# Kernel optimization log

Measured on AMD Instinct MI355X. Metric: run time of the kernel, lower is better.

The kernel has to match this reference:

```python
import jax, jax.numpy as jnp
import numpy as np
import math

N = 100000       # nodes
E = 640000       # edges
VOCAB = 8192
EMB = 96         # node_embedding_dim
SEL = 32         # node_selector_dim
H = EMB + SEL    # hidden_dim = 128
T = 3            # num_edge_types
P = 64           # positional_embedding_dim
MAXPOS = 512     # max_edge_position
ITERS = 6        # ggnn_iterations


def _sinusoidal(max_pos, dim):
    pos = np.arange(max_pos)[:, None].astype(np.float32)
    div = np.exp(np.arange(0, dim, 2).astype(np.float32) * (-math.log(10000.0) / dim))
    pe = np.zeros((max_pos, dim), np.float32)
    pe[:, 0::2] = np.sin(pos * div)
    pe[:, 1::2] = np.cos(pos * div)
    return jnp.asarray(pe)


def setup_inputs() -> dict:
    key = jax.random.key(0)
    ks = jax.random.split(key, 20)
    s = 1.0 / np.sqrt(H).astype(np.float32)
    inp = {
        "x_text_indices": jax.random.randint(ks[0], (N,), 0, VOCAB, dtype=jnp.int32),
        "node_selectors": jax.random.normal(ks[1], (N, SEL), jnp.float32),
        "edge_index": jax.random.randint(ks[2], (2, E), 0, N, dtype=jnp.int32),
        "edge_type": jax.random.randint(ks[3], (E,), 0, T, dtype=jnp.int32),
        "edge_positions": jax.random.randint(ks[4], (E,), 0, MAXPOS + 1, dtype=jnp.int32),
        "emb": (jax.random.normal(ks[5], (VOCAB, EMB), jnp.float32) * 0.02).at[0].set(0.0),  # padding_idx=0
        "pos_enc": _sinusoidal(MAXPOS + 1, P),
        "Wg": jax.random.normal(ks[6], (P, H), jnp.float32) * (1.0 / np.sqrt(P)),
        "bg": jnp.zeros((H,), jnp.float32),
        "Wt": jax.random.normal(ks[7], (T, H, H), jnp.float32) * s,
        "bt": jnp.zeros((T, H), jnp.float32),
        "W_ih": jax.random.normal(ks[8], (3 * H, H), jnp.float32) * s,
        "W_hh": jax.random.normal(ks[9], (3 * H, H), jnp.float32) * s,
        "b_ih": jnp.zeros((3 * H,), jnp.float32),
        "b_hh": jnp.zeros((3 * H,), jnp.float32),
        "W1": jax.random.normal(ks[10], (2 * H, H), jnp.float32) * (1.0 / np.sqrt(2 * H)),
        "b1": jnp.zeros((H,), jnp.float32),
        "W2": jax.random.normal(ks[11], (H, 1), jnp.float32) * s,
        "b2": jnp.zeros((1,), jnp.float32),
    }
    return inp


def _gru_cell(x, h, W_ih, W_hh, b_ih, b_hh):
    # torch.nn.GRUCell math
    gi = x @ W_ih.T + b_ih          # [N, 3H]
    gh = h @ W_hh.T + b_hh          # [N, 3H]
    i_r, i_z, i_n = jnp.split(gi, 3, axis=-1)
    h_r, h_z, h_n = jnp.split(gh, 3, axis=-1)
    r = jax.nn.sigmoid(i_r + h_r)
    z = jax.nn.sigmoid(i_z + h_z)
    n = jnp.tanh(i_n + r * h_n)
    return (1.0 - z) * n + z * h


def reference(x_text_indices, node_selectors, edge_index, edge_type, edge_positions,
              emb, pos_enc, Wg, bg, Wt, bt, W_ih, W_hh, b_ih, b_hh, W1, b1, W2, b2):
    src, dst = edge_index[0], edge_index[1]
    h0 = jnp.concatenate([emb[x_text_indices], node_selectors], axis=-1)  # [N, H]
    pe_e = pos_enc[edge_positions]                                        # [E, P]
    gate = 2.0 * jax.nn.sigmoid(pe_e @ Wg + bg)                           # [E, H]
    cnt = jax.ops.segment_sum(jnp.ones((E,), h0.dtype), dst, num_segments=N)
    denom = jnp.maximum(cnt, 1.0)[:, None]                                # mean-scatter, 0 if no in-edges

    h = h0
    for _ in range(ITERS):
        gx = h[src] * gate                                                # gather + gate [E, H]
        # edge-type routed linear: sum over the one active type per edge
        msg = jnp.zeros_like(gx)
        for t in range(T):
            mask = (edge_type == t)[:, None].astype(gx.dtype)
            msg = msg + mask * (gx @ Wt[t] + bt[t])
        agg = jax.ops.segment_sum(msg, dst, num_segments=N) / denom       # mean aggregation [N, H]
        h = _gru_cell(agg, h, W_ih, W_hh, b_ih, b_hh)

    feats = jnp.concatenate([h, h0], axis=-1)                             # [N, 2H]
    logits = jax.nn.relu(feats @ W1 + b1) @ W2 + b2                       # [N, 1]
    return logits
```

## Files before the change

### kernel.cpp

```cpp
#include <hip/hip_runtime.h>
#include <cstdint>
#include <cstddef>

#define HD 128
#define EMBD 96
#define SELD 32
#define PD 64
#define NPOS 513
#define GITERS 6

typedef _Float16 f16;
typedef __attribute__((ext_vector_type(8))) _Float16 f16x8;
typedef __attribute__((ext_vector_type(4))) _Float16 f16x4;
typedef __attribute__((ext_vector_type(2))) _Float16 f16x2;
typedef __attribute__((ext_vector_type(4))) float f32x4;

__device__ __forceinline__ float sigm(float x) {
    return __builtin_amdgcn_rcpf(1.0f + __expf(-x));
}
__device__ __forceinline__ float tanh_f(float x) {
    return 2.0f * __builtin_amdgcn_rcpf(1.0f + __expf(-2.0f * x)) - 1.0f;
}


__global__ void k_deg(const int* __restrict__ ei, const int* __restrict__ et,
                      int* __restrict__ cnt_t, int E, int N) {
    int e = blockIdx.x * 256 + threadIdx.x;
    if (e < E) {
        int d = ei[E + e];
        atomicAdd(&cnt_t[(size_t)et[e] * N + d], 1);
    }
}

__launch_bounds__(1024)
__global__ void k_scan1(const int* __restrict__ cnt_t, int* __restrict__ rp,
                        int* __restrict__ bsum, int N) {
    __shared__ int sc[1024];
    int t = threadIdx.x;
    int i = blockIdx.x * 1024 + t;
    int v = 0;
    if (i < N)
        v = cnt_t[i] + cnt_t[(size_t)N + i] + cnt_t[2 * (size_t)N + i];
    sc[t] = v;
    __syncthreads();
    for (int off = 1; off < 1024; off <<= 1) {
        int u = (t >= off) ? sc[t - off] : 0;
        __syncthreads();
        sc[t] += u;
        __syncthreads();
    }
    if (i < N) rp[i] = sc[t] - v;
    if (t == 1023) bsum[blockIdx.x] = sc[t];
}

__launch_bounds__(1024)
__global__ void k_scan2(int* __restrict__ bsum, int nb) {
    __shared__ int sc[1024];
    int t = threadIdx.x;
    int v = (t < nb) ? bsum[t] : 0;
    sc[t] = v;
    __syncthreads();
    for (int off = 1; off < 1024; off <<= 1) {
        int u = (t >= off) ? sc[t - off] : 0;
        __syncthreads();
        sc[t] += u;
        __syncthreads();
    }
    if (t < nb) bsum[t] = sc[t] - v;
}

__global__ void k_scan3(const int* __restrict__ rp, const int* __restrict__ bsum,
                        const int* __restrict__ cnt_t, float4* __restrict__ cntp,
                        int4* __restrict__ rp4, int N) {
    int i = blockIdx.x * 256 + threadIdx.x;
    if (i < N) {
        int start = rp[i] + bsum[i >> 10];
        int c0 = cnt_t[i];
        int c1 = cnt_t[(size_t)N + i];
        int c2 = cnt_t[2 * (size_t)N + i];
        rp4[i] = make_int4(start, start + c0, start + c0 + c1, start + c0 + c1 + c2);
        float4 v;
        v.x = (float)c0; v.y = (float)c1; v.z = (float)c2;
        v.w = 1.0f / fmaxf((float)(c0 + c1 + c2), 1.0f);
        cntp[i] = v;
    }
}

__global__ void k_fill(const int* __restrict__ ei, const int* __restrict__ et,
                       const int* __restrict__ ep, const int4* __restrict__ rp4,
                       int* __restrict__ cur3, int2* __restrict__ e2, int E, int N) {
    int e = blockIdx.x * 256 + threadIdx.x;
    if (e < E) {
        int d = ei[E + e];
        int t = et[e];
        int4 r4 = rp4[d];
        int base = (t == 0) ? r4.x : ((t == 1) ? r4.y : r4.z);
        int pos = atomicAdd(&cur3[(size_t)t * N + d], 1);
        e2[base + pos] = make_int2(ei[e], ep[e]);
    }
}

__global__ void k_gate(const float* __restrict__ pe, const float* __restrict__ Wg,
                       const float* __restrict__ bg, f16* __restrict__ gb) {
    int p = blockIdx.x;
    int j = threadIdx.x;
    float acc = bg[j];
    #pragma unroll 8
    for (int k = 0; k < PD; ++k) acc += pe[p * PD + k] * Wg[k * HD + j];
    gb[p * HD + j] = (f16)(2.0f * sigm(acc));
}

__global__ void k_prep(const float* __restrict__ Wt, const float* __restrict__ W1,
                       f16* __restrict__ WtT, f16* __restrict__ W1T) {
    const int SZ = 3 * HD * HD;
    int id = blockIdx.x * 256 + threadIdx.x;
    if (id < SZ) {
        int t = id / (HD * HD), rem = id % (HD * HD);
        int n = rem / HD, k = rem % HD;
        WtT[id] = (f16)Wt[t * HD * HD + k * HD + n];
    } else if (id < SZ + 2 * HD * HD) {
        int rem = id - SZ;
        int n = rem / (2 * HD), k = rem % (2 * HD);
        W1T[rem] = (f16)W1[k * HD + n];
    }
}

__global__ void k_prepW(const float* __restrict__ Wih, const float* __restrict__ Whh,
                        f16* __restrict__ Wcat) {
    int id = blockIdx.x * 256 + threadIdx.x;
    if (id < 512 * 256) {
        int j = id >> 8, k = id & 255;
        float v;
        if (j < 256)      v = (k < 128) ? Wih[j * 128 + k] : Whh[j * 128 + (k - 128)];
        else if (j < 384) v = (k < 128) ? Wih[j * 128 + k] : 0.0f;
        else              v = (k < 128) ? 0.0f : Whh[(j - 128) * 128 + (k - 128)];
        Wcat[id] = (f16)v;
    }
}

__global__ void k_init(const int* __restrict__ xidx, const float* __restrict__ sel,
                       const float* __restrict__ emb, f16* __restrict__ h, int N) {
    int id = blockIdx.x * 256 + threadIdx.x;
    if (id < N * HD) {
        int n = id >> 7, j = id & 127;
        float v = (j < EMBD) ? emb[(size_t)xidx[n] * EMBD + j]
                             : sel[(size_t)n * SELD + (j - EMBD)];
        h[id] = (f16)v;
    }
}

__launch_bounds__(512, 4)
__global__ void k_agg(const int4* __restrict__ rp4, const int2* __restrict__ e2,
                      const f16* __restrict__ h_in, const f16* __restrict__ gb,
                      const f16* __restrict__ WtT, const float* __restrict__ bt,
                      const float4* __restrict__ cntp, f16* __restrict__ agg, int N) {
    __shared__ f16 S[3 * 16 * 136];
    __shared__ f16 aggL[16 * 136];

    int tid = threadIdx.x;
    int wave = tid >> 6, lane = tid & 63;
    int quad = lane >> 4, m = lane & 15;
    int half = lane >> 5, hl = lane & 31;
    int d0 = blockIdx.x * 16;

    {
        int lrow = wave + half * 8;
        int grow = d0 + lrow;
        bool valid = grow < N;
        int4 r4 = rp4[min(grow, N - 1)];
        int es = r4.x, b1 = r4.y, b2 = r4.z, ee = r4.w;
        if (!valid) ee = es;
        int dg = ee - es;
        int dmax = max(dg, __shfl_xor(dg, 32));
        int nb = (__builtin_amdgcn_readfirstlane(dmax) + 7) >> 3;
        int co = hl * 4;

        const f16x4 zf = {0, 0, 0, 0};
        f16x4 accA = zf, accB = zf, accC = zf;
        for (int b = 0; b < nb; ++b) {
            int e0 = es + b * 8;
            int2 ev[8];
            #pragma unroll
            for (int j = 0; j < 8; ++j) {
                int idx = max(min(e0 + j, ee - 1), 0);
                ev[j] = e2[idx];
            }
            f16x4 hv[8], gv[8];
            #pragma unroll
            for (int j = 0; j < 8; ++j) {
                hv[j] = *(const f16x4*)(h_in + (size_t)ev[j].x * HD + co);
                gv[j] = *(const f16x4*)(gb + (size_t)ev[j].y * HD + co);
            }
            #pragma unroll
            for (int j = 0; j < 8; ++j) {
                int eidx = e0 + j;
                f16x4 g0 = (eidx < ee) ? gv[j] : zf;
                accA += hv[j] * g0;
                f16x4 gB = (eidx >= b1) ? g0 : zf;
                accB += hv[j] * gB;
                f16x4 gC = (eidx >= b2) ? g0 : zf;
                accC += hv[j] * gC;
            }
        }
        f16x4 s0 = accA - accB;
        f16x4 s1 = accB - accC;
        *(f16x4*)(S + (0 * 16 + lrow) * 136 + co) = s0;
        *(f16x4*)(S + (1 * 16 + lrow) * 136 + co) = s1;
        *(f16x4*)(S + (2 * 16 + lrow) * 136 + co) = accC;
    }
    __syncthreads();

    {
        int col = wave * 16 + m;
        f32x4 acc = {0.f, 0.f, 0.f, 0.f};
        #pragma unroll
        for (int t = 0; t < 3; ++t)
            #pragma unroll
            for (int c = 0; c < 4; ++c) {
                f16x8 a = *(const f16x8*)(S + (t * 16 + m) * 136 + c * 32 + quad * 8);
                f16x8 b = *(const f16x8*)(WtT + ((size_t)t * HD + col) * HD + c * 32 + quad * 8);
                acc = __builtin_amdgcn_mfma_f32_16x16x32_f16(a, b, acc, 0, 0, 0);
            }
        float bt0 = bt[col], bt1 = bt[HD + col], bt2 = bt[2 * HD + col];
        #pragma unroll
        for (int r = 0; r < 4; ++r) {
            int lr = quad * 4 + r;
            int dd2 = min(d0 + lr, N - 1);
            float4 cp = cntp[dd2];
            float v = (acc[r] + cp.x * bt0 + cp.y * bt1 + cp.z * bt2) * cp.w;
            aggL[lr * 136 + col] = (f16)v;
        }
    }
    __syncthreads();

    {
        int row = tid >> 5, ch = tid & 31;
        if (d0 + row < N) {
            f16x4 v = *(const f16x4*)(aggL + row * 136 + ch * 4);
            *(f16x4*)(agg + (size_t)(d0 + row) * HD + ch * 4) = v;
        }
    }
}

__launch_bounds__(512, 4)
__global__ void k_gru(const f16* __restrict__ agg, const f16* __restrict__ h_in,
                      const f16* __restrict__ Wcat, const float* __restrict__ bih,
                      const float* __restrict__ bhh, f16* __restrict__ h_out, int N) {
    __shared__ f16 AL[64 * 264];

    int tid = threadIdx.x;
    int wave = tid >> 6, lane = tid & 63;
    int quad = lane >> 4, m = lane & 15;
    int d0 = blockIdx.x * 64;

    {
        int rsub = tid >> 5;
        int ch = tid & 31;
        #pragma unroll
        for (int i = 0; i < 4; ++i) {
            int row = i * 16 + rsub;
            int grow = min(d0 + row, N - 1);
            f16x8 v;
            if (ch < 16) v = *(const f16x8*)(agg + (size_t)grow * HD + ch * 8);
            else         v = *(const f16x8*)(h_in + (size_t)grow * HD + (ch - 16) * 8);
            *(f16x8*)(AL + row * 264 + ch * 8) = v;
        }
    }
    __syncthreads();

    int j = wave * 16 + m;
    f32x4 ar[4], az[4], an[4], ah[4];
    const f32x4 z4 = {0.f, 0.f, 0.f, 0.f};
    #pragma unroll
    for (int tau = 0; tau < 4; ++tau) { ar[tau] = z4; az[tau] = z4; an[tau] = z4; ah[tau] = z4; }

    #pragma unroll
    for (int c = 0; c < 8; ++c) {
        f16x8 br = *(const f16x8*)(Wcat + (size_t)j * 256 + c * 32 + quad * 8);
        f16x8 bz = *(const f16x8*)(Wcat + (size_t)(128 + j) * 256 + c * 32 + quad * 8);
        f16x8 bn = (c < 4)
            ? *(const f16x8*)(Wcat + (size_t)(256 + j) * 256 + c * 32 + quad * 8)
            : *(const f16x8*)(Wcat + (size_t)(384 + j) * 256 + c * 32 + quad * 8);
        #pragma unroll
        for (int tau = 0; tau < 4; ++tau) {
            f16x8 a = *(const f16x8*)(AL + (tau * 16 + m) * 264 + c * 32 + quad * 8);
            ar[tau] = __builtin_amdgcn_mfma_f32_16x16x32_f16(a, br, ar[tau], 0, 0, 0);
            az[tau] = __builtin_amdgcn_mfma_f32_16x16x32_f16(a, bz, az[tau], 0, 0, 0);
            if (c < 4) an[tau] = __builtin_amdgcn_mfma_f32_16x16x32_f16(a, bn, an[tau], 0, 0, 0);
            else       ah[tau] = __builtin_amdgcn_mfma_f32_16x16x32_f16(a, bn, ah[tau], 0, 0, 0);
        }
    }

    float b_r  = bih[j] + bhh[j];
    float b_z  = bih[HD + j] + bhh[HD + j];
    float b_in = bih[2 * HD + j];
    float b_hn = bhh[2 * HD + j];
    float hp[4][4];
    #pragma unroll
    for (int tau = 0; tau < 4; ++tau)
        #pragma unroll
        for (int r = 0; r < 4; ++r) {
            int row = tau * 16 + quad * 4 + r;
            float hval = (float)AL[row * 264 + 128 + j];
            float rr = sigm(ar[tau][r] + b_r);
            float zz = sigm(az[tau][r] + b_z);
            float nn = tanh_f(an[tau][r] + b_in + rr * (ah[tau][r] + b_hn));
            hp[tau][r] = (1.0f - zz) * nn + zz * hval;
        }
    __syncthreads();

    #pragma unroll
    for (int tau = 0; tau < 4; ++tau)
        #pragma unroll
        for (int r = 0; r < 4; ++r)
            AL[(tau * 16 + quad * 4 + r) * 132 + j] = (f16)hp[tau][r];
    __syncthreads();

    {
        int rsub = tid >> 5, ch = tid & 31;
        #pragma unroll
        for (int i = 0; i < 4; ++i) {
            int row = i * 16 + rsub;
            if (d0 + row < N) {
                f16x4 v = *(const f16x4*)(AL + row * 132 + ch * 4);
                *(f16x4*)(h_out + (size_t)(d0 + row) * HD + ch * 4) = v;
            }
        }
    }
}

__launch_bounds__(256)
__global__ void k_final(const f16* __restrict__ h_f, const int* __restrict__ xidx,
                        const float* __restrict__ sel, const float* __restrict__ emb,
                        const f16* __restrict__ W1T, const float* __restrict__ b1,
                        const float* __restrict__ W2, const float* __restrict__ b2,
                        float* __restrict__ out, int N) {
    __shared__ float red[4][16];
    int tid = threadIdx.x;
    int wave = tid >> 6, lane = tid & 63;
    int quad = lane >> 4, m = lane & 15;
    int row0 = blockIdx.x * 16;
    int arow = min(row0 + m, N - 1);
    int xi = xidx[arow];

    f16x8 fa[8];
    #pragma unroll
    for (int c = 0; c < 4; ++c)
        fa[c] = *(const f16x8*)(h_f + (size_t)arow * HD + c * 32 + quad * 8);
    #pragma unroll
    for (int c = 4; c < 7; ++c) {
        const float* ep = emb + (size_t)xi * EMBD + (c - 4) * 32 + quad * 8;
        #pragma unroll
        for (int jj = 0; jj < 8; ++jj) fa[c][jj] = (f16)ep[jj];
    }
    {
        const float* sp = sel + (size_t)arow * SELD + quad * 8;
        #pragma unroll
        for (int jj = 0; jj < 8; ++jj) fa[7][jj] = (f16)sp[jj];
    }

    f32x4 acc[2];
    const f32x4 z4 = {0.f, 0.f, 0.f, 0.f};
    acc[0] = z4; acc[1] = z4;
    #pragma unroll
    for (int s = 0; s < 2; ++s) {
        int c0 = (wave * 2 + s) * 16;
        #pragma unroll
        for (int c = 0; c < 8; ++c) {
            f16x8 b = *(const f16x8*)(W1T + (size_t)(c0 + m) * (2 * HD) + c * 32 + quad * 8);
            acc[s] = __builtin_amdgcn_mfma_f32_16x16x32_f16(fa[c], b, acc[s], 0, 0, 0);
        }
    }

    float psum[4] = {0.f, 0.f, 0.f, 0.f};
    #pragma unroll
    for (int s = 0; s < 2; ++s) {
        int col = (wave * 2 + s) * 16 + m;
        float b1v = b1[col], w2v = W2[col];
        #pragma unroll
        for (int r = 0; r < 4; ++r)
            psum[r] += fmaxf(acc[s][r] + b1v, 0.0f) * w2v;
    }
    #pragma unroll
    for (int off = 1; off < 16; off <<= 1)
        #pragma unroll
        for (int r = 0; r < 4; ++r) psum[r] += __shfl_xor(psum[r], off);

    if (m == 0) {
        #pragma unroll
        for (int r = 0; r < 4; ++r) red[wave][quad * 4 + r] = psum[r];
    }
    __syncthreads();
    if (tid < 16) {
        int row = row0 + tid;
        if (row < N) out[row] = red[0][tid] + red[1][tid] + red[2][tid] + red[3][tid] + b2[0];
    }
}


extern "C" void kernel_launch(void* const* d_in, const int* in_sizes, int n_in,
                              void* d_out, int out_size, void* d_ws, size_t ws_size,
                              hipStream_t stream) {
    const int*   xidx = (const int*)d_in[0];
    const float* sel  = (const float*)d_in[1];
    const int*   ei   = (const int*)d_in[2];
    const int*   et   = (const int*)d_in[3];
    const int*   ep   = (const int*)d_in[4];
    const float* emb  = (const float*)d_in[5];
    const float* pe   = (const float*)d_in[6];
    const float* Wg   = (const float*)d_in[7];
    const float* bg   = (const float*)d_in[8];
    const float* Wt   = (const float*)d_in[9];
    const float* bt   = (const float*)d_in[10];
    const float* Wih  = (const float*)d_in[11];
    const float* Whh  = (const float*)d_in[12];
    const float* bih  = (const float*)d_in[13];
    const float* bhh  = (const float*)d_in[14];
    const float* W1   = (const float*)d_in[15];
    const float* b1   = (const float*)d_in[16];
    const float* W2   = (const float*)d_in[17];
    const float* b2   = (const float*)d_in[18];

    const int N = in_sizes[0];
    const int E = in_sizes[3];
    const size_t NH = (size_t)N * HD;

    char* p = (char*)d_ws;
    f16*    hbf0  = (f16*)p;    p += NH * 2;
    f16*    hbf1  = (f16*)p;    p += NH * 2;
    f16*    aggb  = (f16*)p;    p += NH * 2;
    f16*    gb    = (f16*)p;    p += (size_t)NPOS * HD * 2;
    f16*    WtT   = (f16*)p;    p += 3 * HD * HD * 2;
    f16*    Wcat  = (f16*)p;    p += 512 * 256 * 2;
    f16*    W1T   = (f16*)p;    p += 2 * HD * HD * 2;
    float4* cntp  = (float4*)p; p += (size_t)N * 16;
    int4*   rp4   = (int4*)p;   p += (size_t)N * 16;
    int* cnt_t  = (int*)p; p += 3 * (size_t)N * 4;
    int* rp     = (int*)p; p += (size_t)N * 4;
    int* cur3   = (int*)p; p += 3 * (size_t)N * 4;
    int* bsum   = (int*)p; p += 1024 * 4;
    int2* e2    = (int2*)p;

    hipMemsetAsync(cnt_t, 0, 3 * (size_t)N * sizeof(int), stream);
    hipMemsetAsync(cur3, 0, 3 * (size_t)N * sizeof(int), stream);
    k_deg<<<(E + 255) / 256, 256, 0, stream>>>(ei, et, cnt_t, E, N);
    const int nb1 = (N + 1023) / 1024;
    k_scan1<<<nb1, 1024, 0, stream>>>(cnt_t, rp, bsum, N);
    k_scan2<<<1, 1024, 0, stream>>>(bsum, nb1);
    k_scan3<<<(N + 255) / 256, 256, 0, stream>>>(rp, bsum, cnt_t, cntp, rp4, N);
    k_fill<<<(E + 255) / 256, 256, 0, stream>>>(ei, et, ep, rp4, cur3, e2, E, N);
    k_gate<<<NPOS, HD, 0, stream>>>(pe, Wg, bg, gb);
    k_prep<<<(3 * HD * HD + 2 * HD * HD + 255) / 256, 256, 0, stream>>>(Wt, W1, WtT, W1T);
    k_prepW<<<512, 256, 0, stream>>>(Wih, Whh, Wcat);
    k_init<<<(N * HD + 255) / 256, 256, 0, stream>>>(xidx, sel, emb, hbf0, N);

    const int gA = (N + 15) / 16;
    const int gG = (N + 63) / 64;
    const f16* hin = hbf0;
    f16* hout = hbf1;
    for (int it = 0; it < GITERS; ++it) {
        k_agg<<<gA, 512, 0, stream>>>(rp4, e2, hin, gb, WtT, bt, cntp, aggb, N);
        k_gru<<<gG, 512, 0, stream>>>(aggb, hin, Wcat, bih, bhh, hout, N);
        const f16* tmp = hout;
        hout = (f16*)hin;
        hin = tmp;
    }

    const int gF = (N + 15) / 16;
    k_final<<<gF, 256, 0, stream>>>(hin, xidx, sel, emb, W1T, b1, W2, b2, (float*)d_out, N);
}
```

Baseline: 1.353 ms.

## Fuse edge aggregation and GRU update into one per-iteration kernel

Merges k_agg and k_gru into a single k_iter kernel that handles 32 destination rows per block. The aggregated messages stay in LDS and feed the GRU MFMAs directly, so the agg buffer is no longer written to and read back from global memory and one launch per iteration goes away. The gather now uses 16 lanes per row with 8-wide f16 loads. In exchange, each block reads the Wcat weights for only 32 rows instead of 64, and the per-block LDS and register footprint changes.

```diff
diff --git a/kernel.cpp b/kernel.cpp
--- a/kernel.cpp
+++ b/kernel.cpp
@@ -8,6 +8,7 @@
 #define PD 64
 #define NPOS 513
 #define GITERS 6
+#define SROW 136
 
 typedef _Float16 f16;
 typedef __attribute__((ext_vector_type(8))) _Float16 f16x8;
@@ -150,33 +151,43 @@
 }
 
 __launch_bounds__(512, 4)
-__global__ void k_agg(const int4* __restrict__ rp4, const int2* __restrict__ e2,
-                      const f16* __restrict__ h_in, const f16* __restrict__ gb,
-                      const f16* __restrict__ WtT, const float* __restrict__ bt,
-                      const float4* __restrict__ cntp, f16* __restrict__ agg, int N) {
-    __shared__ f16 S[3 * 16 * 136];
-    __shared__ f16 aggL[16 * 136];
+__global__ void k_iter(const int4* __restrict__ rp4, const int2* __restrict__ e2,
+                       const f16* __restrict__ h_in, const f16* __restrict__ gb,
+                       const f16* __restrict__ WtT, const float* __restrict__ bt,
+                       const float4* __restrict__ cntp, const f16* __restrict__ Wcat,
+                       const float* __restrict__ bih, const float* __restrict__ bhh,
+                       f16* __restrict__ h_out, int N) {
+    __shared__ f16 S[3 * 32 * SROW];
+    __shared__ f16 hL[32 * SROW];
 
     int tid = threadIdx.x;
     int wave = tid >> 6, lane = tid & 63;
     int quad = lane >> 4, m = lane & 15;
-    int half = lane >> 5, hl = lane & 31;
-    int d0 = blockIdx.x * 16;
-
-    {
-        int lrow = wave + half * 8;
+    int d0 = blockIdx.x * 32;
+
+    {
+        int row = tid >> 4, ch = tid & 15;
+        int grow = min(d0 + row, N - 1);
+        f16x8 v = *(const f16x8*)(h_in + (size_t)grow * HD + ch * 8);
+        *(f16x8*)(hL + row * SROW + ch * 8) = v;
+    }
+
+    {
+        int qw = lane >> 4, ql = lane & 15;
+        int lrow = wave + qw * 8;
         int grow = d0 + lrow;
         bool valid = grow < N;
         int4 r4 = rp4[min(grow, N - 1)];
         int es = r4.x, b1 = r4.y, b2 = r4.z, ee = r4.w;
         if (!valid) ee = es;
         int dg = ee - es;
-        int dmax = max(dg, __shfl_xor(dg, 32));
-        int nb = (__builtin_amdgcn_readfirstlane(dmax) + 7) >> 3;
-        int co = hl * 4;
-
-        const f16x4 zf = {0, 0, 0, 0};
-        f16x4 accA = zf, accB = zf, accC = zf;
+        int t1 = max(dg, __shfl_xor(dg, 16));
+        int t2 = max(t1, __shfl_xor(t1, 32));
+        int nb = (__builtin_amdgcn_readfirstlane(t2) + 7) >> 3;
+        int co = ql * 8;
+
+        const f16x8 zf = {0, 0, 0, 0, 0, 0, 0, 0};
+        f16x8 accA = zf, accB = zf, accC = zf;
         for (int b = 0; b < nb; ++b) {
             int e0 = es + b * 8;
             int2 ev[8];
@@ -185,146 +196,125 @@
                 int idx = max(min(e0 + j, ee - 1), 0);
                 ev[j] = e2[idx];
             }
-            f16x4 hv[8], gv[8];
+            f16x8 hv[8], gv[8];
             #pragma unroll
             for (int j = 0; j < 8; ++j) {
-                hv[j] = *(const f16x4*)(h_in + (size_t)ev[j].x * HD + co);
-                gv[j] = *(const f16x4*)(gb + (size_t)ev[j].y * HD + co);
+                hv[j] = *(const f16x8*)(h_in + (size_t)ev[j].x * HD + co);
+                gv[j] = *(const f16x8*)(gb + (size_t)ev[j].y * HD + co);
             }
             #pragma unroll
             for (int j = 0; j < 8; ++j) {
                 int eidx = e0 + j;
-                f16x4 g0 = (eidx < ee) ? gv[j] : zf;
+                f16x8 g0 = (eidx < ee) ? gv[j] : zf;
                 accA += hv[j] * g0;
-                f16x4 gB = (eidx >= b1) ? g0 : zf;
+                f16x8 gB = (eidx >= b1) ? g0 : zf;
                 accB += hv[j] * gB;
-                f16x4 gC = (eidx >= b2) ? g0 : zf;
+                f16x8 gC = (eidx >= b2) ? g0 : zf;
                 accC += hv[j] * gC;
             }
         }
-        f16x4 s0 = accA - accB;
-        f16x4 s1 = accB - accC;
-        *(f16x4*)(S + (0 * 16 + lrow) * 136 + co) = s0;
-        *(f16x4*)(S + (1 * 16 + lrow) * 136 + co) = s1;
-        *(f16x4*)(S + (2 * 16 + lrow) * 136 + co) = accC;
-    }
-    __syncthreads();
-
-    {
-        int col = wave * 16 + m;
-        f32x4 acc = {0.f, 0.f, 0.f, 0.f};
-        #pragma unroll
-        for (int t = 0; t < 3; ++t)
-            #pragma unroll
-            for (int c = 0; c < 4; ++c) {
-                f16x8 a = *(const f16x8*)(S + (t * 16 + m) * 136 + c * 32 + quad * 8);
-                f16x8 b = *(const f16x8*)(WtT + ((size_t)t * HD + col) * HD + c * 32 + quad * 8);
-                acc = __builtin_amdgcn_mfma_f32_16x16x32_f16(a, b, acc, 0, 0, 0);
-            }
-        float bt0 = bt[col], bt1 = bt[HD + col], bt2 = bt[2 * HD + col];
-        #pragma unroll
-        for (int r = 0; r < 4; ++r) {
-            int lr = quad * 4 + r;
-            int dd2 = min(d0 + lr, N - 1);
-            float4 cp = cntp[dd2];
-            float v = (acc[r] + cp.x * bt0 + cp.y * bt1 + cp.z * bt2) * cp.w;
-            aggL[lr * 136 + col] = (f16)v;
+        f16x8 s0 = accA - accB;
+        f16x8 s1 = accB - accC;
+        *(f16x8*)(S + (0 * 32 + lrow) * SROW + co) = s0;
+        *(f16x8*)(S + (1 * 32 + lrow) * SROW + co) = s1;
+        *(f16x8*)(S + (2 * 32 + lrow) * SROW + co) = accC;
+    }
+    __syncthreads();
+
+    float aggv[2][4];
+    {
+        int tau = wave & 1, cgp = wave >> 1;
+        #pragma unroll
+        for (int s = 0; s < 2; ++s) {
+            int col = cgp * 32 + s * 16 + m;
+            f32x4 acc = {0.f, 0.f, 0.f, 0.f};
+            #pragma unroll
+            for (int t = 0; t < 3; ++t)
+                #pragma unroll
+                for (int c = 0; c < 4; ++c) {
+                    f16x8 a = *(const f16x8*)(S + (t * 32 + tau * 16 + m) * SROW + c * 32 + quad * 8);
+                    f16x8 b = *(const f16x8*)(WtT + ((size_t)t * HD + col) * HD + c * 32 + quad * 8);
+                    acc = __builtin_amdgcn_mfma_f32_16x16x32_f16(a, b, acc, 0, 0, 0);
+                }
+            float bt0 = bt[col], bt1 = bt[HD + col], bt2 = bt[2 * HD + col];
+            #pragma unroll
+            for (int r = 0; r < 4; ++r) {
+                int lr = tau * 16 + quad * 4 + r;
+                int dd = min(d0 + lr, N - 1);
+                float4 cp = cntp[dd];
+                aggv[s][r] = (acc[r] + cp.x * bt0 + cp.y * bt1 + cp.z * bt2) * cp.w;
+            }
         }
     }
     __syncthreads();
 
     {
-        int row = tid >> 5, ch = tid & 31;
+        int tau = wave & 1, cgp = wave >> 1;
+        #pragma unroll
+        for (int s = 0; s < 2; ++s)
+            #pragma unroll
+            for (int r = 0; r < 4; ++r)
+                S[(tau * 16 + quad * 4 + r) * SROW + cgp * 32 + s * 16 + m] = (f16)aggv[s][r];
+    }
+    __syncthreads();
+
+    {
+        int j = wave * 16 + m;
+        f32x4 ar[2], az[2], an[2], ah[2];
+        const f32x4 z4 = {0.f, 0.f, 0.f, 0.f};
+        #pragma unroll
+        for (int t2 = 0; t2 < 2; ++t2) { ar[t2] = z4; az[t2] = z4; an[t2] = z4; ah[t2] = z4; }
+
+        #pragma unroll
+        for (int c = 0; c < 8; ++c) {
+            f16x8 br = *(const f16x8*)(Wcat + (size_t)j * 256 + c * 32 + quad * 8);
+            f16x8 bz = *(const f16x8*)(Wcat + (size_t)(128 + j) * 256 + c * 32 + quad * 8);
+            f16x8 bn = (c < 4)
+                ? *(const f16x8*)(Wcat + (size_t)(256 + j) * 256 + c * 32 + quad * 8)
+                : *(const f16x8*)(Wcat + (size_t)(384 + j) * 256 + c * 32 + quad * 8);
+            #pragma unroll
+            for (int t2 = 0; t2 < 2; ++t2) {
+                f16x8 a = (c < 4)
+                    ? *(const f16x8*)(S + (t2 * 16 + m) * SROW + c * 32 + quad * 8)
+                    : *(const f16x8*)(hL + (t2 * 16 + m) * SROW + (c - 4) * 32 + quad * 8);
+                ar[t2] = __builtin_amdgcn_mfma_f32_16x16x32_f16(a, br, ar[t2], 0, 0, 0);
+                az[t2] = __builtin_amdgcn_mfma_f32_16x16x32_f16(a, bz, az[t2], 0, 0, 0);
+                if (c < 4) an[t2] = __builtin_amdgcn_mfma_f32_16x16x32_f16(a, bn, an[t2], 0, 0, 0);
+                else       ah[t2] = __builtin_amdgcn_mfma_f32_16x16x32_f16(a, bn, ah[t2], 0, 0, 0);
+            }
+        }
+
+        float b_r  = bih[j] + bhh[j];
+        float b_z  = bih[HD + j] + bhh[HD + j];
+        float b_in = bih[2 * HD + j];
+        float b_hn = bhh[2 * HD + j];
+        float hp[2][4];
+        #pragma unroll
+        for (int t2 = 0; t2 < 2; ++t2)
+            #pragma unroll
+            for (int r = 0; r < 4; ++r) {
+                int row = t2 * 16 + quad * 4 + r;
+                float hval = (float)hL[row * SROW + j];
+                float rr = sigm(ar[t2][r] + b_r);
+                float zz = sigm(az[t2][r] + b_z);
+                float nn = tanh_f(an[t2][r] + b_in + rr * (ah[t2][r] + b_hn));
+                hp[t2][r] = (1.0f - zz) * nn + zz * hval;
+            }
+        __syncthreads();
+
+        #pragma unroll
+        for (int t2 = 0; t2 < 2; ++t2)
+            #pragma unroll
+            for (int r = 0; r < 4; ++r)
+                S[(t2 * 16 + quad * 4 + r) * SROW + j] = (f16)hp[t2][r];
+    }
+    __syncthreads();
+
+    {
+        int row = tid >> 4, ch = tid & 15;
         if (d0 + row < N) {
-            f16x4 v = *(const f16x4*)(aggL + row * 136 + ch * 4);
-            *(f16x4*)(agg + (size_t)(d0 + row) * HD + ch * 4) = v;
-        }
-    }
-}
-
-__launch_bounds__(512, 4)
-__global__ void k_gru(const f16* __restrict__ agg, const f16* __restrict__ h_in,
-                      const f16* __restrict__ Wcat, const float* __restrict__ bih,
-                      const float* __restrict__ bhh, f16* __restrict__ h_out, int N) {
-    __shared__ f16 AL[64 * 264];
-
-    int tid = threadIdx.x;
-    int wave = tid >> 6, lane = tid & 63;
-    int quad = lane >> 4, m = lane & 15;
-    int d0 = blockIdx.x * 64;
-
-    {
-        int rsub = tid >> 5;
-        int ch = tid & 31;
-        #pragma unroll
-        for (int i = 0; i < 4; ++i) {
-            int row = i * 16 + rsub;
-            int grow = min(d0 + row, N - 1);
-            f16x8 v;
-            if (ch < 16) v = *(const f16x8*)(agg + (size_t)grow * HD + ch * 8);
-            else         v = *(const f16x8*)(h_in + (size_t)grow * HD + (ch - 16) * 8);
-            *(f16x8*)(AL + row * 264 + ch * 8) = v;
-        }
-    }
-    __syncthreads();
-
-    int j = wave * 16 + m;
-    f32x4 ar[4], az[4], an[4], ah[4];
-    const f32x4 z4 = {0.f, 0.f, 0.f, 0.f};
-    #pragma unroll
-    for (int tau = 0; tau < 4; ++tau) { ar[tau] = z4; az[tau] = z4; an[tau] = z4; ah[tau] = z4; }
-
-    #pragma unroll
-    for (int c = 0; c < 8; ++c) {
-        f16x8 br = *(const f16x8*)(Wcat + (size_t)j * 256 + c * 32 + quad * 8);
-        f16x8 bz = *(const f16x8*)(Wcat + (size_t)(128 + j) * 256 + c * 32 + quad * 8);
-        f16x8 bn = (c < 4)
-            ? *(const f16x8*)(Wcat + (size_t)(256 + j) * 256 + c * 32 + quad * 8)
-            : *(const f16x8*)(Wcat + (size_t)(384 + j) * 256 + c * 32 + quad * 8);
-        #pragma unroll
-        for (int tau = 0; tau < 4; ++tau) {
-            f16x8 a = *(const f16x8*)(AL + (tau * 16 + m) * 264 + c * 32 + quad * 8);
-            ar[tau] = __builtin_amdgcn_mfma_f32_16x16x32_f16(a, br, ar[tau], 0, 0, 0);
-            az[tau] = __builtin_amdgcn_mfma_f32_16x16x32_f16(a, bz, az[tau], 0, 0, 0);
-            if (c < 4) an[tau] = __builtin_amdgcn_mfma_f32_16x16x32_f16(a, bn, an[tau], 0, 0, 0);
-            else       ah[tau] = __builtin_amdgcn_mfma_f32_16x16x32_f16(a, bn, ah[tau], 0, 0, 0);
-        }
-    }
-
-    float b_r  = bih[j] + bhh[j];
-    float b_z  = bih[HD + j] + bhh[HD + j];
-    float b_in = bih[2 * HD + j];
-    float b_hn = bhh[2 * HD + j];
-    float hp[4][4];
-    #pragma unroll
-    for (int tau = 0; tau < 4; ++tau)
-        #pragma unroll
-        for (int r = 0; r < 4; ++r) {
-            int row = tau * 16 + quad * 4 + r;
-            float hval = (float)AL[row * 264 + 128 + j];
-            float rr = sigm(ar[tau][r] + b_r);
-            float zz = sigm(az[tau][r] + b_z);
-            float nn = tanh_f(an[tau][r] + b_in + rr * (ah[tau][r] + b_hn));
-            hp[tau][r] = (1.0f - zz) * nn + zz * hval;
-        }
-    __syncthreads();
-
-    #pragma unroll
-    for (int tau = 0; tau < 4; ++tau)
-        #pragma unroll
-        for (int r = 0; r < 4; ++r)
-            AL[(tau * 16 + quad * 4 + r) * 132 + j] = (f16)hp[tau][r];
-    __syncthreads();
-
-    {
-        int rsub = tid >> 5, ch = tid & 31;
-        #pragma unroll
-        for (int i = 0; i < 4; ++i) {
-            int row = i * 16 + rsub;
-            if (d0 + row < N) {
-                f16x4 v = *(const f16x4*)(AL + row * 132 + ch * 4);
-                *(f16x4*)(h_out + (size_t)(d0 + row) * HD + ch * 4) = v;
-            }
+            f16x8 v = *(const f16x8*)(S + row * SROW + ch * 8);
+            *(f16x8*)(h_out + (size_t)(d0 + row) * HD + ch * 8) = v;
         }
     }
 }
@@ -428,7 +418,6 @@
     char* p = (char*)d_ws;
     f16*    hbf0  = (f16*)p;    p += NH * 2;
     f16*    hbf1  = (f16*)p;    p += NH * 2;
-    f16*    aggb  = (f16*)p;    p += NH * 2;
     f16*    gb    = (f16*)p;    p += (size_t)NPOS * HD * 2;
     f16*    WtT   = (f16*)p;    p += 3 * HD * HD * 2;
     f16*    Wcat  = (f16*)p;    p += 512 * 256 * 2;
@@ -454,13 +443,12 @@
     k_prepW<<<512, 256, 0, stream>>>(Wih, Whh, Wcat);
     k_init<<<(N * HD + 255) / 256, 256, 0, stream>>>(xidx, sel, emb, hbf0, N);
 
-    const int gA = (N + 15) / 16;
-    const int gG = (N + 63) / 64;
+    const int gI = (N + 31) / 32;
     const f16* hin = hbf0;
     f16* hout = hbf1;
     for (int it = 0; it < GITERS; ++it) {
-        k_agg<<<gA, 512, 0, stream>>>(rp4, e2, hin, gb, WtT, bt, cntp, aggb, N);
-        k_gru<<<gG, 512, 0, stream>>>(aggb, hin, Wcat, bih, bhh, hout, N);
+        k_iter<<<gI, 512, 0, stream>>>(rp4, e2, hin, gb, WtT, bt, cntp, Wcat,
+                                       bih, bhh, hout, N);
         const f16* tmp = hout;
         hout = (f16*)hin;
         hin = tmp;
```

After: 1.408 ms. 4.1% more time.
